# Performance work log

Hardware: AMD Instinct MI355X
Metric: run time of the kernel (lower is better)

Reference implementation:

```python
import jax, jax.numpy as jnp
import numpy as np

GAMMA = 1.0
EPS = 1e-06
MAXITERS = 100


def setup_inputs() -> dict:
    key = jax.random.key(0)
    B, H, W = 64, 512, 512
    M = jax.random.uniform(key, (B, H, W), dtype=jnp.float32)
    return {"M": M}


def reference(M):
    """Entropy-regularized OT via Sinkhorn with uniform marginals (r=c=None path).

    Matches torch loop: row-normalize, check col marginal convergence, break
    BEFORE col-normalizing if converged, else col-normalize.
    """
    B, H, W = M.shape
    r = jnp.full((1, H), 1.0 / H, dtype=M.dtype)
    c = jnp.full((1, W), 1.0 / W, dtype=M.dtype)
    P0 = jnp.exp(-GAMMA * M)

    def cond(state):
        i, P, done = state
        return jnp.logical_and(i < MAXITERS, jnp.logical_not(done))

    def body(state):
        i, P, _ = state
        alpha = P.sum(axis=2)                      # (B,H)
        P = (r / alpha)[:, :, None] * P            # row normalize
        beta = P.sum(axis=1)                       # (B,W)
        done = jnp.all(jnp.abs(beta - c) <= EPS)   # isclose(atol=eps, rtol=0)
        # if converged, keep row-normalized P (torch breaks before col scale)
        P = jnp.where(done, P, P * (c / beta)[:, None, :])
        return i + 1, P, done

    _, P, _ = jax.lax.while_loop(cond, body, (jnp.int32(0), P0, jnp.array(False)))
    return P
```

## Files before the change

### kernel.cpp

```cpp
#include <hip/hip_runtime.h>
#include <hip/hip_fp16.h>
#include <hip/hip_cooperative_groups.h>
#include <cstddef>

namespace cg = cooperative_groups;

#define BATCH 64
#define HW 512
#define RVAL (1.0f / 512.0f)
#define EPS_ 1e-6f
#define MAXIT 100
#define NBLK 256
#define NTHR 1024

__device__ __forceinline__ unsigned h2u(__half2 h) {
    union { __half2 h; unsigned u; } c; c.h = h; return c.u;
}
__device__ __forceinline__ __half2 u2h(unsigned u) {
    union { unsigned u; __half2 h; } c; c.u = u; return c.h;
}

__global__ __launch_bounds__(NTHR, 4)
void sinkhorn_lds(const float* __restrict__ M, float* __restrict__ P,
                  float* __restrict__ colpart, int* __restrict__ bar,
                  int tail_mode) {
    const int tid  = threadIdx.x;
    const int bid  = blockIdx.x;
    const int b    = bid >> 2;
    const int slab = bid & 3;
    const int w    = tid >> 6;
    const int l    = tid & 63;

    cg::grid_group grid = cg::this_grid();

    __shared__ unsigned K_lds[128][HW / 2];
    __shared__ float    part[8][HW];
    __shared__ float    v_lds[HW];

    if (tid < HW) v_lds[tid] = 1.0f;
    __syncthreads();

    const float4* Mb = (const float4*)(M + ((size_t)b * HW + slab * 128) * HW);

    float u_loc[8];
    for (int it = 0; it < MAXIT; ++it) {
        float4 v0 = *(const float4*)&v_lds[l * 4];
        float4 v1 = *(const float4*)&v_lds[256 + l * 4];
        float4 cp0 = make_float4(0.f, 0.f, 0.f, 0.f);
        float4 cp1 = make_float4(0.f, 0.f, 0.f, 0.f);

        if (it == 0) {
#pragma unroll
            for (int rr = 0; rr < 8; ++rr) {
                const int row = w * 8 + rr;
                const float4* mp = Mb + (size_t)row * 128;
                float4 m0 = mp[l];
                float4 m1 = mp[64 + l];
                float4 k0, k1;
                k0.x = __expf(-m0.x); k0.y = __expf(-m0.y);
                k0.z = __expf(-m0.z); k0.w = __expf(-m0.w);
                k1.x = __expf(-m1.x); k1.y = __expf(-m1.y);
                k1.z = __expf(-m1.z); k1.w = __expf(-m1.w);
                uint2 q0, q1;
                q0.x = h2u(__floats2half2_rn(k0.x, k0.y));
                q0.y = h2u(__floats2half2_rn(k0.z, k0.w));
                q1.x = h2u(__floats2half2_rn(k1.x, k1.y));
                q1.y = h2u(__floats2half2_rn(k1.z, k1.w));
                *(uint2*)&K_lds[row][2 * l]       = q0;
                *(uint2*)&K_lds[row][128 + 2 * l] = q1;
                float s = k0.x * v0.x + k0.y * v0.y + k0.z * v0.z + k0.w * v0.w
                        + k1.x * v1.x + k1.y * v1.y + k1.z * v1.z + k1.w * v1.w;
#pragma unroll
                for (int off = 32; off >= 1; off >>= 1)
                    s += __shfl_xor(s, off, 64);
                float u = RVAL / s;
                u_loc[rr] = u;
                cp0.x += u * k0.x; cp0.y += u * k0.y;
                cp0.z += u * k0.z; cp0.w += u * k0.w;
                cp1.x += u * k1.x; cp1.y += u * k1.y;
                cp1.z += u * k1.z; cp1.w += u * k1.w;
            }
        } else {
#pragma unroll
            for (int rr = 0; rr < 8; ++rr) {
                const int row = w * 8 + rr;
                uint2 q0 = *(const uint2*)&K_lds[row][2 * l];
                uint2 q1 = *(const uint2*)&K_lds[row][128 + 2 * l];
                float2 a0 = __half22float2(u2h(q0.x));
                float2 a1 = __half22float2(u2h(q0.y));
                float2 b0 = __half22float2(u2h(q1.x));
                float2 b1 = __half22float2(u2h(q1.y));
                float s = a0.x * v0.x + a0.y * v0.y + a1.x * v0.z + a1.y * v0.w
                        + b0.x * v1.x + b0.y * v1.y + b1.x * v1.z + b1.y * v1.w;
#pragma unroll
                for (int off = 32; off >= 1; off >>= 1)
                    s += __shfl_xor(s, off, 64);
                float u = RVAL / s;
                u_loc[rr] = u;
                cp0.x += u * a0.x; cp0.y += u * a0.y;
                cp0.z += u * a1.x; cp0.w += u * a1.y;
                cp1.x += u * b0.x; cp1.y += u * b0.y;
                cp1.z += u * b1.x; cp1.w += u * b1.y;
            }
        }

        if (w < 8) {
            *(float4*)&part[w][l * 4]       = cp0;
            *(float4*)&part[w][256 + l * 4] = cp1;
        }
        __syncthreads();
        if (w >= 8) {
            float4 e0 = *(float4*)&part[w - 8][l * 4];
            float4 e1 = *(float4*)&part[w - 8][256 + l * 4];
            e0.x += cp0.x; e0.y += cp0.y; e0.z += cp0.z; e0.w += cp0.w;
            e1.x += cp1.x; e1.y += cp1.y; e1.z += cp1.z; e1.w += cp1.w;
            *(float4*)&part[w - 8][l * 4]       = e0;
            *(float4*)&part[w - 8][256 + l * 4] = e1;
        }
        __syncthreads();

        float* slot = colpart + ((size_t)((it & 1) * NBLK + bid)) * HW;
        if (tid < HW) {
            float t = 0.f;
#pragma unroll
            for (int ww = 0; ww < 8; ++ww) t += part[ww][tid];
            __hip_atomic_store(&slot[tid], t, __ATOMIC_RELAXED,
                               __HIP_MEMORY_SCOPE_AGENT);
        }
        __syncthreads();

        int* bs = bar + b * MAXIT + it;
        if (tid == 0) {
            __hip_atomic_fetch_add(bs, 1, __ATOMIC_RELAXED,
                                   __HIP_MEMORY_SCOPE_AGENT);
            while (__hip_atomic_load(bs, __ATOMIC_RELAXED,
                                     __HIP_MEMORY_SCOPE_AGENT) < 4)
                __builtin_amdgcn_s_sleep(4);
        }
        __syncthreads();

        float tt = 0.f;
        int viol = 0;
        if (tid < HW) {
            const float* basep =
                colpart + ((size_t)((it & 1) * NBLK + b * 4)) * HW;
#pragma unroll
            for (int bb = 0; bb < 4; ++bb)
                tt += __hip_atomic_load(basep + bb * HW + tid, __ATOMIC_RELAXED,
                                        __HIP_MEMORY_SCOPE_AGENT);
            viol = fabsf(v_lds[tid] * tt - RVAL) > EPS_;
        }
        int any = __syncthreads_or(viol);
        if (!any) break;
        if (tid < HW) v_lds[tid] = RVAL / tt;
        __syncthreads();
    }

    if (tail_mode) grid.sync();

    float4 fv0 = *(const float4*)&v_lds[l * 4];
    float4 fv1 = *(const float4*)&v_lds[256 + l * 4];
    float4* Pb = (float4*)(P + ((size_t)b * HW + slab * 128) * HW);
#pragma unroll
    for (int rr = 0; rr < 8; ++rr) {
        const int row = w * 8 + rr;
        float u = u_loc[rr];
        uint2 q0 = *(const uint2*)&K_lds[row][2 * l];
        uint2 q1 = *(const uint2*)&K_lds[row][128 + 2 * l];
        float2 a0 = __half22float2(u2h(q0.x));
        float2 a1 = __half22float2(u2h(q0.y));
        float2 b0 = __half22float2(u2h(q1.x));
        float2 b1 = __half22float2(u2h(q1.y));
        float4 o0, o1;
        o0.x = u * a0.x * fv0.x; o0.y = u * a0.y * fv0.y;
        o0.z = u * a1.x * fv0.z; o0.w = u * a1.y * fv0.w;
        o1.x = u * b0.x * fv1.x; o1.y = u * b0.y * fv1.y;
        o1.z = u * b1.x * fv1.z; o1.w = u * b1.y * fv1.w;
        Pb[(size_t)row * 128 + l]      = o0;
        Pb[(size_t)row * 128 + 64 + l] = o1;
    }
}

extern "C" void kernel_launch(void* const* d_in, const int* in_sizes, int n_in,
                              void* d_out, int out_size, void* d_ws, size_t ws_size,
                              hipStream_t stream) {
    const float* M = (const float*)d_in[0];
    float* P = (float*)d_out;

    const size_t CP_BYTES  = (size_t)2 * NBLK * HW * sizeof(float);
    const size_t BAR_BYTES = (size_t)BATCH * MAXIT * sizeof(int);
    const size_t NEED = CP_BYTES + BAR_BYTES;

    char* scratch;
    int tail_mode;
    if (ws_size >= NEED) {
        scratch = (char*)d_ws;
        tail_mode = 0;
    } else {
        scratch = (char*)d_out + (size_t)out_size * sizeof(float) - NEED;
        tail_mode = 1;
    }
    float* colpart = (float*)scratch;
    int*   bar     = (int*)(scratch + CP_BYTES);

    hipMemsetAsync(bar, 0, BAR_BYTES, stream);

    void* args[] = { (void*)&M, (void*)&P, (void*)&colpart, (void*)&bar,
                     (void*)&tail_mode };
    hipLaunchCooperativeKernel((const void*)sinkhorn_lds, dim3(NBLK),
                               dim3(NTHR), args, 0, stream);
}
```

Baseline: 65.55 us.

## Cut block barriers per Sinkhorn iteration with per-wave arrivals and double-buffered v

Each of the 8 storing waves now publishes its column partials, waits for its own stores, and bumps the per-batch counter itself (target 32 instead of 4). Every wave polls the counter independently instead of relying on thread 0 plus two __syncthreads. The column scale vector is double-buffered so the new v can be written before the OR-reduction, which drops another barrier. Nontemporal loads for M and nontemporal stores for P are also added. The cost is more atomic traffic and polling from many waves, and correctness now depends on per-wave vmcnt ordering under relaxed atomics.

```diff
diff --git a/kernel.cpp b/kernel.cpp
--- a/kernel.cpp
+++ b/kernel.cpp
@@ -13,6 +13,8 @@
 #define NBLK 256
 #define NTHR 1024
 
+typedef float f32x4 __attribute__((ext_vector_type(4)));
+
 __device__ __forceinline__ unsigned h2u(__half2 h) {
     union { __half2 h; unsigned u; } c; c.h = h; return c.u;
 }
@@ -21,9 +23,9 @@
 }
 
 __global__ __launch_bounds__(NTHR, 4)
-void sinkhorn_lds(const float* __restrict__ M, float* __restrict__ P,
-                  float* __restrict__ colpart, int* __restrict__ bar,
-                  int tail_mode) {
+void sinkhorn_lds2(const float* __restrict__ M, float* __restrict__ P,
+                   float* __restrict__ colpart, int* __restrict__ bar,
+                   int tail_mode) {
     const int tid  = threadIdx.x;
     const int bid  = blockIdx.x;
     const int b    = bid >> 2;
@@ -35,17 +37,19 @@
 
     __shared__ unsigned K_lds[128][HW / 2];
     __shared__ float    part[8][HW];
-    __shared__ float    v_lds[HW];
-
-    if (tid < HW) v_lds[tid] = 1.0f;
+    __shared__ float    v_lds[2][HW];
+
+    if (tid < HW) v_lds[0][tid] = 1.0f;
     __syncthreads();
 
-    const float4* Mb = (const float4*)(M + ((size_t)b * HW + slab * 128) * HW);
+    const f32x4* Mb =
+        (const f32x4*)(M + ((size_t)b * HW + slab * 128) * HW);
 
     float u_loc[8];
+    int cur = 0;
     for (int it = 0; it < MAXIT; ++it) {
-        float4 v0 = *(const float4*)&v_lds[l * 4];
-        float4 v1 = *(const float4*)&v_lds[256 + l * 4];
+        float4 v0 = *(const float4*)&v_lds[cur][l * 4];
+        float4 v1 = *(const float4*)&v_lds[cur][256 + l * 4];
         float4 cp0 = make_float4(0.f, 0.f, 0.f, 0.f);
         float4 cp1 = make_float4(0.f, 0.f, 0.f, 0.f);
 
@@ -53,9 +57,9 @@
 #pragma unroll
             for (int rr = 0; rr < 8; ++rr) {
                 const int row = w * 8 + rr;
-                const float4* mp = Mb + (size_t)row * 128;
-                float4 m0 = mp[l];
-                float4 m1 = mp[64 + l];
+                const f32x4* mp = Mb + (size_t)row * 128;
+                f32x4 m0 = __builtin_nontemporal_load(mp + l);
+                f32x4 m1 = __builtin_nontemporal_load(mp + 64 + l);
                 float4 k0, k1;
                 k0.x = __expf(-m0.x); k0.y = __expf(-m0.y);
                 k0.z = __expf(-m0.z); k0.w = __expf(-m0.w);
@@ -120,24 +124,25 @@
         __syncthreads();
 
         float* slot = colpart + ((size_t)((it & 1) * NBLK + bid)) * HW;
-        if (tid < HW) {
+        int* bs = bar + b * MAXIT + it;
+        if (w < 8) {
+            const int col = w * 64 + l;
             float t = 0.f;
 #pragma unroll
-            for (int ww = 0; ww < 8; ++ww) t += part[ww][tid];
-            __hip_atomic_store(&slot[tid], t, __ATOMIC_RELAXED,
+            for (int ww = 0; ww < 8; ++ww) t += part[ww][col];
+            __hip_atomic_store(&slot[col], t, __ATOMIC_RELAXED,
                                __HIP_MEMORY_SCOPE_AGENT);
-        }
-        __syncthreads();
-
-        int* bs = bar + b * MAXIT + it;
-        if (tid == 0) {
-            __hip_atomic_fetch_add(bs, 1, __ATOMIC_RELAXED,
-                                   __HIP_MEMORY_SCOPE_AGENT);
+            asm volatile("s_waitcnt vmcnt(0)" ::: "memory");
+            if (l == 0)
+                __hip_atomic_fetch_add(bs, 1, __ATOMIC_RELAXED,
+                                       __HIP_MEMORY_SCOPE_AGENT);
+        }
+
+        if (l == 0) {
             while (__hip_atomic_load(bs, __ATOMIC_RELAXED,
-                                     __HIP_MEMORY_SCOPE_AGENT) < 4)
-                __builtin_amdgcn_s_sleep(4);
-        }
-        __syncthreads();
+                                     __HIP_MEMORY_SCOPE_AGENT) < 32)
+                __builtin_amdgcn_s_sleep(1);
+        }
 
         float tt = 0.f;
         int viol = 0;
@@ -148,19 +153,19 @@
             for (int bb = 0; bb < 4; ++bb)
                 tt += __hip_atomic_load(basep + bb * HW + tid, __ATOMIC_RELAXED,
                                         __HIP_MEMORY_SCOPE_AGENT);
-            viol = fabsf(v_lds[tid] * tt - RVAL) > EPS_;
+            viol = fabsf(v_lds[cur][tid] * tt - RVAL) > EPS_;
+            v_lds[cur ^ 1][tid] = RVAL / tt;
         }
         int any = __syncthreads_or(viol);
         if (!any) break;
-        if (tid < HW) v_lds[tid] = RVAL / tt;
-        __syncthreads();
+        cur ^= 1;
     }
 
     if (tail_mode) grid.sync();
 
-    float4 fv0 = *(const float4*)&v_lds[l * 4];
-    float4 fv1 = *(const float4*)&v_lds[256 + l * 4];
-    float4* Pb = (float4*)(P + ((size_t)b * HW + slab * 128) * HW);
+    float4 fv0 = *(const float4*)&v_lds[cur][l * 4];
+    float4 fv1 = *(const float4*)&v_lds[cur][256 + l * 4];
+    f32x4* Pb = (f32x4*)(P + ((size_t)b * HW + slab * 128) * HW);
 #pragma unroll
     for (int rr = 0; rr < 8; ++rr) {
         const int row = w * 8 + rr;
@@ -171,13 +176,13 @@
         float2 a1 = __half22float2(u2h(q0.y));
         float2 b0 = __half22float2(u2h(q1.x));
         float2 b1 = __half22float2(u2h(q1.y));
-        float4 o0, o1;
+        f32x4 o0, o1;
         o0.x = u * a0.x * fv0.x; o0.y = u * a0.y * fv0.y;
         o0.z = u * a1.x * fv0.z; o0.w = u * a1.y * fv0.w;
         o1.x = u * b0.x * fv1.x; o1.y = u * b0.y * fv1.y;
         o1.z = u * b1.x * fv1.z; o1.w = u * b1.y * fv1.w;
-        Pb[(size_t)row * 128 + l]      = o0;
-        Pb[(size_t)row * 128 + 64 + l] = o1;
+        __builtin_nontemporal_store(o0, Pb + (size_t)row * 128 + l);
+        __builtin_nontemporal_store(o1, Pb + (size_t)row * 128 + 64 + l);
     }
 }
 
@@ -207,6 +212,6 @@
 
     void* args[] = { (void*)&M, (void*)&P, (void*)&colpart, (void*)&bar,
                      (void*)&tail_mode };
-    hipLaunchCooperativeKernel((const void*)sinkhorn_lds, dim3(NBLK),
+    hipLaunchCooperativeKernel((const void*)sinkhorn_lds2, dim3(NBLK),
                                dim3(NTHR), args, 0, stream);
 }
```

New measurement: 71.49 us. 9.1% more time.
